# Kernel tuning notes

Hardware: AMD Instinct MI355X
Metric: run time of the kernel (lower is better)

## Reference

```python
import jax, jax.numpy as jnp
import numpy as np

LOG_DT_MIN, LOG_DT_MAX = np.log(0.001), np.log(0.1)


def setup_inputs() -> dict:
    L, H, P = 8192, 512, 256
    key = jax.random.key(0)
    ks = jax.random.split(key, 8)
    # continuous-time diagonal state matrix: Re < 0 for stability (HiPPO-like)
    Lambda_re = -(0.1 + jax.random.uniform(ks[0], (P,), dtype=jnp.float32))
    Lambda_im = jnp.pi * jax.random.normal(ks[1], (P,), dtype=jnp.float32)
    # B ~ Vinv @ B_init stored as (...,2) real/imag; C ~ C_init @ V likewise
    B = jax.random.normal(ks[2], (P, H, 2), dtype=jnp.float32) / np.sqrt(2.0 * P)
    C = jax.random.normal(ks[3], (H, P, 2), dtype=jnp.float32) / np.sqrt(2.0 * P)
    D = jax.random.normal(ks[4], (H,), dtype=jnp.float32)
    log_step = (jax.random.uniform(ks[5], (P,), dtype=jnp.float32)
                * (LOG_DT_MAX - LOG_DT_MIN) + LOG_DT_MIN)
    input_sequence = jax.random.normal(ks[6], (L, H), dtype=jnp.float32)
    hidden = jnp.zeros((1, P), dtype=jnp.float32)  # initial state (real part; imag 0)
    resets = jax.random.randint(ks[7], (L,), 0, 2, dtype=jnp.int32)
    return dict(hidden=hidden, input_sequence=input_sequence, Lambda_re=Lambda_re,
                Lambda_im=Lambda_im, B=B, C=C, D=D, log_step=log_step, resets=resets)


def _binary_operator_reset(q_i, q_j):
    A_i, b_i, c_i = q_i
    A_j, b_j, c_j = q_j
    return (A_j * A_i * (1 - c_j) + A_j * c_j,
            (A_j * b_i + b_j) * (1 - c_j) + b_j * c_j,
            c_i * (1 - c_j) + c_j)


def reference(hidden, input_sequence, Lambda_re, Lambda_im, B, C, D, log_step, resets):
    # S5SSM forward: zoh discretization, conj_sym=True, step_rescale=1.0
    Lambda = (Lambda_re + 1j * Lambda_im).astype(jnp.complex64)           # (P,)
    B_tilde = (B[..., 0] + 1j * B[..., 1]).astype(jnp.complex64)          # (P,H)
    C_tilde = (C[..., 0] + 1j * C[..., 1]).astype(jnp.complex64)          # (H,P)
    step = jnp.exp(log_step)                                              # (P,)
    # zero-order-hold discretization
    Lambda_bar = jnp.exp(Lambda * step)                                   # (P,)
    B_bar = ((Lambda_bar - 1.0) / Lambda)[:, None] * B_tilde              # (P,H)

    L, P = input_sequence.shape[0], Lambda.shape[0]
    Bu = input_sequence.astype(jnp.complex64) @ B_bar.T                   # (L,P)
    Lambda_elems = jnp.concatenate(
        [jnp.ones((1, P), Lambda_bar.dtype), jnp.broadcast_to(Lambda_bar, (L, P))])
    Bu_elems = jnp.concatenate([hidden.astype(jnp.complex64), Bu])        # (L+1,P)
    r = jnp.concatenate([jnp.zeros((1,), jnp.float32),
                         resets.astype(jnp.float32)])[:, None]            # (L+1,1)

    _, xs, _ = jax.lax.associative_scan(_binary_operator_reset,
                                        (Lambda_elems, Bu_elems, r))
    xs = xs[1:]                                                           # (L,P)
    ys = 2.0 * (xs @ C_tilde.T).real                                      # conj_sym factor 2, (L,H)
    out = ys + input_sequence * D                                         # feedthrough Du
    return out
```

## Files before the change

kernel.cpp:

```cpp
#include <hip/hip_runtime.h>

#define L_LEN 8192
#define H_DIM 512
#define P_DIM 256
#define N2P   512
#define CHUNKS 512
#define CLEN  (L_LEN / CHUNKS)

typedef short bf16x8 __attribute__((ext_vector_type(8)));
typedef float f32x4  __attribute__((ext_vector_type(4)));

#define OFF_BMT   0
#define OFF_W2T   (OFF_BMT + 131072)
#define OFF_LBRE  (OFF_W2T + 131072)
#define OFF_LBIM  (OFF_LBRE + 256)
#define OFF_BU    (OFF_LBIM + 256)
#define OFF_XC    (OFF_BU + 2097152)
#define OFF_AGAR  (OFF_XC + 2097152)
#define OFF_AGAI  (OFF_AGAR + CHUNKS * P_DIM)
#define OFF_AGBR  (OFF_AGAI + CHUNKS * P_DIM)
#define OFF_AGBI  (OFF_AGBR + CHUNKS * P_DIM)
#define OFF_AGC   (OFF_AGBI + CHUNKS * P_DIM)
#define OFF_CARR  (OFF_AGC  + CHUNKS)
#define OFF_CARI  (OFF_CARR + CHUNKS * P_DIM)

__device__ __forceinline__ unsigned short bfr(float x) {
    unsigned u = __float_as_uint(x);
    u = (u + 0x7fffu + ((u >> 16) & 1u)) >> 16;
    return (unsigned short)u;
}
__device__ __forceinline__ unsigned pk(float a, float b) {
    return (unsigned)bfr(a) | ((unsigned)bfr(b) << 16);
}
__device__ __forceinline__ float b2f(unsigned short v) {
    return __uint_as_float(((unsigned)v) << 16);
}
__device__ __forceinline__ void gl2lds16(const void* g, void* l) {
    __builtin_amdgcn_global_load_lds(
        (const __attribute__((address_space(1))) void*)g,
        (__attribute__((address_space(3))) void*)l, 16, 0, 0);
}

__global__ __launch_bounds__(256) void s5_k0(
    const float* __restrict__ Lre, const float* __restrict__ Lim,
    const float* __restrict__ logstep,
    const float* __restrict__ B,
    const float* __restrict__ C,
    short* __restrict__ BmT, unsigned* __restrict__ W2Tu,
    float* __restrict__ Lbre, float* __restrict__ Lbim)
{
    int idx = blockIdx.x * 256 + threadIdx.x;

    int p = idx >> 9, h = idx & 511;
    float lre = Lre[p], lim = Lim[p];
    float s = expf(logstep[p]);
    float er = expf(lre * s);
    float lbr = er * cosf(lim * s);
    float lbi = er * sinf(lim * s);
    if (h == 0) { Lbre[p] = lbr; Lbim[p] = lbi; }
    float nr = lbr - 1.0f, ni = lbi;
    float inv = 1.0f / (lre * lre + lim * lim);
    float fr = (nr * lre + ni * lim) * inv;
    float fi = (ni * lre - nr * lim) * inv;
    float b0 = B[2 * idx + 0];
    float b1 = B[2 * idx + 1];
    BmT[(size_t)p * 512 + h]         = (short)bfr(fr * b0 - fi * b1);
    BmT[(size_t)(256 + p) * 512 + h] = (short)bfr(fr * b1 + fi * b0);

    int hh = idx >> 8, pp = idx & 255;
    float cre = C[2 * idx + 0];
    float cim = C[2 * idx + 1];
    W2Tu[(size_t)hh * 256 + pp] = pk(2.0f * cre, -2.0f * cim);
}

template<bool AFP32, bool EPI>
__global__ __launch_bounds__(512) void s5_gemm(
    const void* __restrict__ Ap, const short* __restrict__ WT,
    const float* __restrict__ u, const float* __restrict__ Dv,
    void* __restrict__ Outp)
{
    __shared__ __align__(16) short sA[2][64][64];
    __shared__ __align__(16) short sB[2][256][64];

    const int tid = threadIdx.x;
    const int bid = blockIdx.x;
    const int rowBase = (bid & 127) * 64;
    const int colBase = (bid >> 7) * 256;

    const int w = tid >> 6, l = tid & 63;
    const int wr = (w >> 2) * 32, wc = (w & 3) * 64;
    const int fr = l & 15, fq = l >> 4;

    float4 fa[2];
    f32x4 acc[2][4] = {};

    auto STAGE_B = [&](int bf, int t) {
        const int kk = t * 64;
        #pragma unroll
        for (int i = 0; i < 4; ++i) {
            int e = i * 512 + tid;
            int row = e >> 3, c8 = (e & 7) << 3;
            gl2lds16(WT + (size_t)(colBase + row) * 512 + kk + c8, &sB[bf][row][c8]);
        }
    };
    auto STAGE_A16 = [&](int bf, int t) {
        const int kk = t * 64;
        const short* A = (const short*)Ap;
        int row = tid >> 3, c8 = (tid & 7) << 3;
        gl2lds16(A + (size_t)(rowBase + row) * 512 + kk + c8, &sA[bf][row][c8]);
    };
    auto LOADA_REG = [&](int t) {
        const int kk = t * 64;
        const float* A = (const float*)Ap;
        int row = tid >> 3, c8 = (tid & 7) << 3;
        const float4* s = (const float4*)(A + (size_t)(rowBase + row) * 512 + kk + c8);
        fa[0] = s[0]; fa[1] = s[1];
    };
    auto CONVA_WRITE = [&](int bf) {
        int row = tid >> 3, c8 = (tid & 7) << 3;
        int4 wv = make_int4((int)pk(fa[0].x, fa[0].y), (int)pk(fa[0].z, fa[0].w),
                            (int)pk(fa[1].x, fa[1].y), (int)pk(fa[1].z, fa[1].w));
        *(int4*)&sA[bf][row][c8] = wv;
    };
    auto COMPUTE = [&](int bf) {
        #pragma unroll
        for (int kc = 0; kc < 2; ++kc) {
            bf16x8 av[2], bv[4];
            #pragma unroll
            for (int i = 0; i < 2; ++i)
                av[i] = *(const bf16x8*)&sA[bf][wr + 16 * i + fr][kc * 32 + 8 * fq];
            #pragma unroll
            for (int j = 0; j < 4; ++j)
                bv[j] = *(const bf16x8*)&sB[bf][wc + 16 * j + fr][kc * 32 + 8 * fq];
            #pragma unroll
            for (int i = 0; i < 2; ++i)
                #pragma unroll
                for (int j = 0; j < 4; ++j)
                    acc[i][j] = __builtin_amdgcn_mfma_f32_16x16x32_bf16(av[i], bv[j], acc[i][j], 0, 0, 0);
        }
    };

    if (AFP32) { LOADA_REG(0); CONVA_WRITE(0); } else { STAGE_A16(0, 0); }
    STAGE_B(0, 0);
    __syncthreads();

    for (int t = 0; t < 8; ++t) {
        const int cur = t & 1, nxt = cur ^ 1;
        if (t < 7) {
            STAGE_B(nxt, t + 1);
            if (AFP32) LOADA_REG(t + 1); else STAGE_A16(nxt, t + 1);
        }
        COMPUTE(cur);
        if (AFP32 && t < 7) CONVA_WRITE(nxt);
        __syncthreads();
    }

    if (AFP32) {
        unsigned short* Out = (unsigned short*)Outp;
        #pragma unroll
        for (int i = 0; i < 2; ++i)
            #pragma unroll
            for (int j = 0; j < 4; ++j)
                #pragma unroll
                for (int q = 0; q < 4; ++q) {
                    int r = rowBase + wr + 16 * i + fq * 4 + q;
                    int c = colBase + wc + 16 * j + fr;
                    Out[(size_t)r * 512 + c] = bfr(acc[i][j][q]);
                }
    } else {
        float* Out = (float*)Outp;
        float dj[4];
        #pragma unroll
        for (int j = 0; j < 4; ++j) dj[j] = EPI ? Dv[colBase + wc + 16 * j + fr] : 0.f;
        #pragma unroll
        for (int i = 0; i < 2; ++i)
            #pragma unroll
            for (int j = 0; j < 4; ++j)
                #pragma unroll
                for (int q = 0; q < 4; ++q) {
                    int r = rowBase + wr + 16 * i + fq * 4 + q;
                    int c = colBase + wc + 16 * j + fr;
                    float v = acc[i][j][q];
                    if (EPI) v += u[(size_t)r * 512 + c] * dj[j];
                    Out[(size_t)r * 512 + c] = v;
                }
    }
}

__global__ __launch_bounds__(P_DIM) void s5_k2(
    const unsigned short* __restrict__ Bu, const int* __restrict__ resets,
    const float* __restrict__ Lbre, const float* __restrict__ Lbim,
    float* __restrict__ aAr, float* __restrict__ aAi,
    float* __restrict__ aBr, float* __restrict__ aBi, float* __restrict__ aC)
{
    const int p = threadIdx.x, ci = blockIdx.x;
    const float lbr = Lbre[p], lbi = Lbim[p];
    float Ar = 1.f, Ai = 0.f, br = 0.f, bi = 0.f;
    int c = 0;
    const int t0 = ci * CLEN;
    for (int t = t0; t < t0 + CLEN; ++t) {
        int rs = resets[t];
        float bur = b2f(Bu[(size_t)t * 512 + p]);
        float bui = b2f(Bu[(size_t)t * 512 + 256 + p]);
        if (rs) { Ar = lbr; Ai = lbi; br = bur; bi = bui; c = 1; }
        else {
            float nAr = lbr * Ar - lbi * Ai; Ai = lbr * Ai + lbi * Ar; Ar = nAr;
            float nbr = lbr * br - lbi * bi + bur; bi = lbr * bi + lbi * br + bui; br = nbr;
        }
    }
    aAr[ci * P_DIM + p] = Ar; aAi[ci * P_DIM + p] = Ai;
    aBr[ci * P_DIM + p] = br; aBi[ci * P_DIM + p] = bi;
    if (p == 0) aC[ci] = (float)c;
}

__global__ __launch_bounds__(CHUNKS) void s5_k3p(
    const float* __restrict__ hidden,
    const float* __restrict__ aAr, const float* __restrict__ aAi,
    const float* __restrict__ aBr, const float* __restrict__ aBi,
    const float* __restrict__ aC,
    float* __restrict__ carR, float* __restrict__ carI)
{
    __shared__ float sAr[CHUNKS], sAi[CHUNKS], sBr[CHUNKS], sBi[CHUNKS], sC[CHUNKS];
    const int p = blockIdx.x, t = threadIdx.x;

    float Ar = aAr[t * P_DIM + p], Ai = aAi[t * P_DIM + p];
    float br = aBr[t * P_DIM + p], bi = aBi[t * P_DIM + p];
    float c  = aC[t];
    sAr[t] = Ar; sAi[t] = Ai; sBr[t] = br; sBi[t] = bi; sC[t] = c;
    __syncthreads();

    for (int s = 1; s < CHUNKS; s <<= 1) {
        float pAr = 0.f, pAi = 0.f, pBr = 0.f, pBi = 0.f, pC = 0.f;
        const bool has = (t >= s);
        if (has) { pAr = sAr[t-s]; pAi = sAi[t-s]; pBr = sBr[t-s]; pBi = sBi[t-s]; pC = sC[t-s]; }
        __syncthreads();
        if (has) {
            if (c <= 0.5f) {
                float nAr = Ar * pAr - Ai * pAi;
                float nAi = Ar * pAi + Ai * pAr;
                float nbr = Ar * pBr - Ai * pBi + br;
                float nbi = Ar * pBi + Ai * pBr + bi;
                Ar = nAr; Ai = nAi; br = nbr; bi = nbi; c = pC;
            }
            sAr[t] = Ar; sAi[t] = Ai; sBr[t] = br; sBi[t] = bi; sC[t] = c;
        }
        __syncthreads();
    }

    const float h = hidden[p];
    float sr, si;
    if (t == 0) { sr = h; si = 0.f; }
    else {
        float gAr = sAr[t-1], gAi = sAi[t-1], gBr = sBr[t-1], gBi = sBi[t-1], gC = sC[t-1];
        if (gC > 0.5f) { sr = gBr; si = gBi; }
        else           { sr = gAr * h + gBr; si = gAi * h + gBi; }
    }
    carR[t * P_DIM + p] = sr;
    carI[t * P_DIM + p] = si;
}

__global__ __launch_bounds__(P_DIM) void s5_k4(
    const unsigned short* __restrict__ Bu, const int* __restrict__ resets,
    const float* __restrict__ Lbre, const float* __restrict__ Lbim,
    const float* __restrict__ carR, const float* __restrict__ carI,
    unsigned* __restrict__ xcu)
{
    const int p = threadIdx.x, ci = blockIdx.x;
    const float lbr = Lbre[p], lbi = Lbim[p];
    float sr = carR[ci * P_DIM + p];
    float si = carI[ci * P_DIM + p];
    const int t0 = ci * CLEN;
    for (int t = t0; t < t0 + CLEN; ++t) {
        int rs = resets[t];
        float bur = b2f(Bu[(size_t)t * 512 + p]);
        float bui = b2f(Bu[(size_t)t * 512 + 256 + p]);
        if (rs) { sr = bur; si = bui; }
        else {
            float nr = lbr * sr - lbi * si + bur;
            si = lbr * si + lbi * sr + bui;
            sr = nr;
        }
        xcu[(size_t)t * 256 + p] = pk(sr, si);
    }
}

extern "C" void kernel_launch(void* const* d_in, const int* in_sizes, int n_in,
                              void* d_out, int out_size, void* d_ws, size_t ws_size,
                              hipStream_t stream)
{
    const float* hidden  = (const float*)d_in[0];
    const float* u       = (const float*)d_in[1];
    const float* Lre     = (const float*)d_in[2];
    const float* Lim     = (const float*)d_in[3];
    const float* B       = (const float*)d_in[4];
    const float* C       = (const float*)d_in[5];
    const float* D       = (const float*)d_in[6];
    const float* logstep = (const float*)d_in[7];
    const int*   resets  = (const int*)d_in[8];
    float* out = (float*)d_out;
    float* ws  = (float*)d_ws;

    short*          BmT  = (short*)(ws + OFF_BMT);
    short*          W2T  = (short*)(ws + OFF_W2T);
    unsigned*       W2Tu = (unsigned*)(ws + OFF_W2T);
    float*          Lbre = ws + OFF_LBRE;
    float*          Lbim = ws + OFF_LBIM;
    unsigned short* Bu   = (unsigned short*)(ws + OFF_BU);
    short*          xc   = (short*)(ws + OFF_XC);
    unsigned*       xcu  = (unsigned*)(ws + OFF_XC);

    s5_k0<<<512, 256, 0, stream>>>(Lre, Lim, logstep, B, C, BmT, W2Tu, Lbre, Lbim);

    s5_gemm<true, false><<<256, 512, 0, stream>>>(
        (const void*)u, BmT, nullptr, nullptr, (void*)Bu);

    s5_k2<<<CHUNKS, P_DIM, 0, stream>>>(Bu, resets, Lbre, Lbim,
        ws + OFF_AGAR, ws + OFF_AGAI, ws + OFF_AGBR, ws + OFF_AGBI, ws + OFF_AGC);

    s5_k3p<<<P_DIM, CHUNKS, 0, stream>>>(hidden,
        ws + OFF_AGAR, ws + OFF_AGAI, ws + OFF_AGBR, ws + OFF_AGBI, ws + OFF_AGC,
        ws + OFF_CARR, ws + OFF_CARI);

    s5_k4<<<CHUNKS, P_DIM, 0, stream>>>(Bu, resets, Lbre, Lbim,
        ws + OFF_CARR, ws + OFF_CARI, xcu);

    s5_gemm<false, true><<<256, 512, 0, stream>>>(
        (const void*)xc, W2T, u, D, (void*)out);
}
```

Measured before the change: 62.26 us.

## Fuse chunk aggregate scan into first GEMM epilogue with interleaved Bu layout

Interleaves the real and imaginary rows of the B projection weights so each GEMM output tile holds paired complex Bu values. The first GEMM now stages its bf16 tile in shared memory, writes it out with coalesced vector stores, and computes the per-chunk scan aggregates from shared memory directly. This removes the separate aggregate kernel and its re-read of Bu from global memory. The GEMM tiles are reshaped to 32 rows with 256 threads and twice as many blocks, and the later scan kernel reads packed 32-bit complex values. The cost is more blocks with less reuse of the B operand per block, and a serial 16-step scan per thread inside the GEMM tail.

```diff
diff --git a/kernel.cpp b/kernel.cpp
--- a/kernel.cpp
+++ b/kernel.cpp
@@ -3,7 +3,6 @@
 #define L_LEN 8192
 #define H_DIM 512
 #define P_DIM 256
-#define N2P   512
 #define CHUNKS 512
 #define CLEN  (L_LEN / CHUNKS)
 
@@ -64,8 +63,8 @@
     float fi = (ni * lre - nr * lim) * inv;
     float b0 = B[2 * idx + 0];
     float b1 = B[2 * idx + 1];
-    BmT[(size_t)p * 512 + h]         = (short)bfr(fr * b0 - fi * b1);
-    BmT[(size_t)(256 + p) * 512 + h] = (short)bfr(fr * b1 + fi * b0);
+    BmT[(size_t)(2 * p) * 512 + h]     = (short)bfr(fr * b0 - fi * b1);
+    BmT[(size_t)(2 * p + 1) * 512 + h] = (short)bfr(fr * b1 + fi * b0);
 
     int hh = idx >> 8, pp = idx & 255;
     float cre = C[2 * idx + 0];
@@ -73,22 +72,26 @@
     W2Tu[(size_t)hh * 256 + pp] = pk(2.0f * cre, -2.0f * cim);
 }
 
-template<bool AFP32, bool EPI>
-__global__ __launch_bounds__(512) void s5_gemm(
+template<bool AFP32, bool EPI, bool AGG>
+__global__ __launch_bounds__(256) void s5_gemm(
     const void* __restrict__ Ap, const short* __restrict__ WT,
     const float* __restrict__ u, const float* __restrict__ Dv,
-    void* __restrict__ Outp)
-{
-    __shared__ __align__(16) short sA[2][64][64];
+    void* __restrict__ Outp,
+    const int* __restrict__ resets,
+    const float* __restrict__ Lbre, const float* __restrict__ Lbim,
+    float* __restrict__ aAr, float* __restrict__ aAi,
+    float* __restrict__ aBr, float* __restrict__ aBi, float* __restrict__ aC)
+{
+    __shared__ __align__(16) short sA[2][32][64];
     __shared__ __align__(16) short sB[2][256][64];
 
     const int tid = threadIdx.x;
     const int bid = blockIdx.x;
-    const int rowBase = (bid & 127) * 64;
-    const int colBase = (bid >> 7) * 256;
+    const int rowBase = (bid & 255) * 32;
+    const int colBase = (bid >> 8) * 256;
 
     const int w = tid >> 6, l = tid & 63;
-    const int wr = (w >> 2) * 32, wc = (w & 3) * 64;
+    const int wc = w * 64;
     const int fr = l & 15, fq = l >> 4;
 
     float4 fa[2];
@@ -97,8 +100,8 @@
     auto STAGE_B = [&](int bf, int t) {
         const int kk = t * 64;
         #pragma unroll
-        for (int i = 0; i < 4; ++i) {
-            int e = i * 512 + tid;
+        for (int i = 0; i < 8; ++i) {
+            int e = i * 256 + tid;
             int row = e >> 3, c8 = (e & 7) << 3;
             gl2lds16(WT + (size_t)(colBase + row) * 512 + kk + c8, &sB[bf][row][c8]);
         }
@@ -128,7 +131,7 @@
             bf16x8 av[2], bv[4];
             #pragma unroll
             for (int i = 0; i < 2; ++i)
-                av[i] = *(const bf16x8*)&sA[bf][wr + 16 * i + fr][kc * 32 + 8 * fq];
+                av[i] = *(const bf16x8*)&sA[bf][16 * i + fr][kc * 32 + 8 * fq];
             #pragma unroll
             for (int j = 0; j < 4; ++j)
                 bv[j] = *(const bf16x8*)&sB[bf][wc + 16 * j + fr][kc * 32 + 8 * fq];
@@ -156,61 +159,74 @@
     }
 
     if (AFP32) {
-        unsigned short* Out = (unsigned short*)Outp;
+        short (*sE)[256] = (short(*)[256])(&sB[0][0][0]);
+        #pragma unroll
+        for (int i = 0; i < 2; ++i)
+            #pragma unroll
+            for (int j = 0; j < 4; ++j)
+                #pragma unroll
+                for (int q = 0; q < 4; ++q)
+                    sE[16 * i + 4 * fq + q][wc + 16 * j + fr] = (short)bfr(acc[i][j][q]);
+        __syncthreads();
+
+        {
+            unsigned short* Out = (unsigned short*)Outp;
+            int row = tid >> 3, c32 = (tid & 7) * 32;
+            unsigned short* gp = Out + (size_t)(rowBase + row) * 512 + colBase + c32;
+            int4 v0 = *(int4*)&sE[row][c32];
+            int4 v1 = *(int4*)&sE[row][c32 + 8];
+            int4 v2 = *(int4*)&sE[row][c32 + 16];
+            int4 v3 = *(int4*)&sE[row][c32 + 24];
+            *(int4*)&gp[0]  = v0;
+            *(int4*)&gp[8]  = v1;
+            *(int4*)&gp[16] = v2;
+            *(int4*)&gp[24] = v3;
+        }
+
+        if (AGG) {
+            const unsigned* sEu = (const unsigned*)(&sB[0][0][0]);
+            int cil = tid >> 7;
+            int pl  = tid & 127;
+            int p   = (colBase >> 1) + pl;
+            const float lbr = Lbre[p], lbi = Lbim[p];
+            float Ar = 1.f, Ai = 0.f, br = 0.f, bi = 0.f;
+            int c = 0;
+            const int r0 = cil * 16;
+            #pragma unroll 4
+            for (int r = r0; r < r0 + 16; ++r) {
+                int rs = resets[rowBase + r];
+                unsigned v = sEu[r * 128 + pl];
+                float bur = b2f((unsigned short)(v & 0xffffu));
+                float bui = b2f((unsigned short)(v >> 16));
+                if (rs) { Ar = lbr; Ai = lbi; br = bur; bi = bui; c = 1; }
+                else {
+                    float nAr = lbr * Ar - lbi * Ai; Ai = lbr * Ai + lbi * Ar; Ar = nAr;
+                    float nbr = lbr * br - lbi * bi + bur; bi = lbr * bi + lbi * br + bui; br = nbr;
+                }
+            }
+            int ci = (rowBase >> 4) + cil;
+            aAr[ci * P_DIM + p] = Ar; aAi[ci * P_DIM + p] = Ai;
+            aBr[ci * P_DIM + p] = br; aBi[ci * P_DIM + p] = bi;
+            if (pl == 0) aC[ci] = (float)c;
+        }
+    } else {
+        float* Out = (float*)Outp;
+        float dj[4];
+        #pragma unroll
+        for (int j = 0; j < 4; ++j) dj[j] = EPI ? Dv[colBase + wc + 16 * j + fr] : 0.f;
         #pragma unroll
         for (int i = 0; i < 2; ++i)
             #pragma unroll
             for (int j = 0; j < 4; ++j)
                 #pragma unroll
                 for (int q = 0; q < 4; ++q) {
-                    int r = rowBase + wr + 16 * i + fq * 4 + q;
-                    int c = colBase + wc + 16 * j + fr;
-                    Out[(size_t)r * 512 + c] = bfr(acc[i][j][q]);
-                }
-    } else {
-        float* Out = (float*)Outp;
-        float dj[4];
-        #pragma unroll
-        for (int j = 0; j < 4; ++j) dj[j] = EPI ? Dv[colBase + wc + 16 * j + fr] : 0.f;
-        #pragma unroll
-        for (int i = 0; i < 2; ++i)
-            #pragma unroll
-            for (int j = 0; j < 4; ++j)
-                #pragma unroll
-                for (int q = 0; q < 4; ++q) {
-                    int r = rowBase + wr + 16 * i + fq * 4 + q;
+                    int r = rowBase + 16 * i + fq * 4 + q;
                     int c = colBase + wc + 16 * j + fr;
                     float v = acc[i][j][q];
                     if (EPI) v += u[(size_t)r * 512 + c] * dj[j];
                     Out[(size_t)r * 512 + c] = v;
                 }
     }
-}
-
-__global__ __launch_bounds__(P_DIM) void s5_k2(
-    const unsigned short* __restrict__ Bu, const int* __restrict__ resets,
-    const float* __restrict__ Lbre, const float* __restrict__ Lbim,
-    float* __restrict__ aAr, float* __restrict__ aAi,
-    float* __restrict__ aBr, float* __restrict__ aBi, float* __restrict__ aC)
-{
-    const int p = threadIdx.x, ci = blockIdx.x;
-    const float lbr = Lbre[p], lbi = Lbim[p];
-    float Ar = 1.f, Ai = 0.f, br = 0.f, bi = 0.f;
-    int c = 0;
-    const int t0 = ci * CLEN;
-    for (int t = t0; t < t0 + CLEN; ++t) {
-        int rs = resets[t];
-        float bur = b2f(Bu[(size_t)t * 512 + p]);
-        float bui = b2f(Bu[(size_t)t * 512 + 256 + p]);
-        if (rs) { Ar = lbr; Ai = lbi; br = bur; bi = bui; c = 1; }
-        else {
-            float nAr = lbr * Ar - lbi * Ai; Ai = lbr * Ai + lbi * Ar; Ar = nAr;
-            float nbr = lbr * br - lbi * bi + bur; bi = lbr * bi + lbi * br + bui; br = nbr;
-        }
-    }
-    aAr[ci * P_DIM + p] = Ar; aAi[ci * P_DIM + p] = Ai;
-    aBr[ci * P_DIM + p] = br; aBi[ci * P_DIM + p] = bi;
-    if (p == 0) aC[ci] = (float)c;
 }
 
 __global__ __launch_bounds__(CHUNKS) void s5_k3p(
@@ -260,7 +276,7 @@
 }
 
 __global__ __launch_bounds__(P_DIM) void s5_k4(
-    const unsigned short* __restrict__ Bu, const int* __restrict__ resets,
+    const unsigned* __restrict__ Bu32, const int* __restrict__ resets,
     const float* __restrict__ Lbre, const float* __restrict__ Lbim,
     const float* __restrict__ carR, const float* __restrict__ carI,
     unsigned* __restrict__ xcu)
@@ -272,8 +288,9 @@
     const int t0 = ci * CLEN;
     for (int t = t0; t < t0 + CLEN; ++t) {
         int rs = resets[t];
-        float bur = b2f(Bu[(size_t)t * 512 + p]);
-        float bui = b2f(Bu[(size_t)t * 512 + 256 + p]);
+        unsigned v = Bu32[(size_t)t * 256 + p];
+        float bur = b2f((unsigned short)(v & 0xffffu));
+        float bui = b2f((unsigned short)(v >> 16));
         if (rs) { sr = bur; si = bui; }
         else {
             float nr = lbr * sr - lbi * si + bur;
@@ -300,30 +317,30 @@
     float* out = (float*)d_out;
     float* ws  = (float*)d_ws;
 
-    short*          BmT  = (short*)(ws + OFF_BMT);
-    short*          W2T  = (short*)(ws + OFF_W2T);
-    unsigned*       W2Tu = (unsigned*)(ws + OFF_W2T);
-    float*          Lbre = ws + OFF_LBRE;
-    float*          Lbim = ws + OFF_LBIM;
-    unsigned short* Bu   = (unsigned short*)(ws + OFF_BU);
-    short*          xc   = (short*)(ws + OFF_XC);
-    unsigned*       xcu  = (unsigned*)(ws + OFF_XC);
+    short*     BmT  = (short*)(ws + OFF_BMT);
+    short*     W2T  = (short*)(ws + OFF_W2T);
+    unsigned*  W2Tu = (unsigned*)(ws + OFF_W2T);
+    float*     Lbre = ws + OFF_LBRE;
+    float*     Lbim = ws + OFF_LBIM;
+    unsigned*  Bu32 = (unsigned*)(ws + OFF_BU);
+    short*     xc   = (short*)(ws + OFF_XC);
+    unsigned*  xcu  = (unsigned*)(ws + OFF_XC);
 
     s5_k0<<<512, 256, 0, stream>>>(Lre, Lim, logstep, B, C, BmT, W2Tu, Lbre, Lbim);
 
-    s5_gemm<true, false><<<256, 512, 0, stream>>>(
-        (const void*)u, BmT, nullptr, nullptr, (void*)Bu);
-
-    s5_k2<<<CHUNKS, P_DIM, 0, stream>>>(Bu, resets, Lbre, Lbim,
+    s5_gemm<true, false, true><<<512, 256, 0, stream>>>(
+        (const void*)u, BmT, nullptr, nullptr, (void*)Bu32,
+        resets, Lbre, Lbim,
         ws + OFF_AGAR, ws + OFF_AGAI, ws + OFF_AGBR, ws + OFF_AGBI, ws + OFF_AGC);
 
     s5_k3p<<<P_DIM, CHUNKS, 0, stream>>>(hidden,
         ws + OFF_AGAR, ws + OFF_AGAI, ws + OFF_AGBR, ws + OFF_AGBI, ws + OFF_AGC,
         ws + OFF_CARR, ws + OFF_CARI);
 
-    s5_k4<<<CHUNKS, P_DIM, 0, stream>>>(Bu, resets, Lbre, Lbim,
+    s5_k4<<<CHUNKS, P_DIM, 0, stream>>>(Bu32, resets, Lbre, Lbim,
         ws + OFF_CARR, ws + OFF_CARI, xcu);
 
-    s5_gemm<false, true><<<256, 512, 0, stream>>>(
-        (const void*)xc, W2T, u, D, (void*)out);
-}
+    s5_gemm<false, true, false><<<512, 256, 0, stream>>>(
+        (const void*)xc, W2T, u, D, (void*)out,
+        nullptr, nullptr, nullptr, nullptr, nullptr, nullptr, nullptr, nullptr);
+}
```

New measurement: 60.17 us. -3.4%, faster.
